# Performance work log

Measured on AMD Instinct MI355X. Metric: run time of the kernel, lower is better.

## Reference

```python
import jax, jax.numpy as jnp
import numpy as np

B, S, IN_DIM = 2048, 65, 256
H, L = 8, 256


def setup_inputs() -> dict:
    key = jax.random.key(0)
    ks = jax.random.split(key, 8)
    return {
        "x": jax.random.normal(ks[0], (B, S, IN_DIM), dtype=jnp.float32),
        "Wq": jax.random.normal(ks[1], (H, IN_DIM, L), dtype=jnp.float32),
        "Wk": jax.random.normal(ks[2], (H, IN_DIM, L), dtype=jnp.float32),
        "Wv": jax.random.normal(ks[3], (H, IN_DIM, L), dtype=jnp.float32),
        "W": jax.random.normal(ks[4], (H, L, 1), dtype=jnp.float32),
        "O": jax.random.normal(ks[5], (H * L, IN_DIM), dtype=jnp.float32),
        "P": jax.random.normal(ks[6], (S - 1, IN_DIM), dtype=jnp.float32),
        "bias": jax.random.normal(ks[7], (H,), dtype=jnp.float32),
    }


def reference(x, Wq, Wk, Wv, W, O, P, bias):
    origin = x[:, 0, :]                       # [B, D]
    walk = x[:, 1:, :]                        # [B, S-1, D]
    origin_seq = origin[:, None, :] + P       # [B, S-1, D]

    # per-head sigmoid projections, vectorized over heads
    k = jax.nn.sigmoid(jnp.einsum('bsd,hdl->bhsl', origin_seq, Wk))
    q = jax.nn.sigmoid(jnp.einsum('bsd,hdl->bhsl', walk, Wq))
    v = jax.nn.sigmoid(jnp.einsum('bsd,hdl->bhsl', walk, Wv))

    edge = jnp.cos(k * q) + bias[None, :, None, None]       # [B,H,S-1,L]
    score = jnp.einsum('bhsl,hl->bhs', edge, W[..., 0])      # [B,H,S-1]
    score = jax.nn.softmax(score, axis=-1)
    res = jnp.einsum('bhs,bhsl->bhl', score, v)              # [B,H,L]
    res = res.reshape(res.shape[0], H * L)                   # concat heads
    out = jax.nn.sigmoid(res @ O)                            # [B, D]
    return jnp.concatenate([out, origin], axis=-1)           # [B, 2D]
```

## Files before the change

### kernel.cpp

```cpp
#include <hip/hip_runtime.h>
#include <math.h>

#define NB   2048
#define NSEQ 65
#define ND   256
#define NH   8
#define NL   256
#define NS   64
#define APAD 264

typedef _Float16 f16;
typedef _Float16 f16x4 __attribute__((ext_vector_type(4)));
typedef _Float16 f16x8 __attribute__((ext_vector_type(8)));
typedef float    f32x4 __attribute__((ext_vector_type(4)));

__device__ __forceinline__ float sigmoidf_(float x) {
    return __builtin_amdgcn_rcpf(1.0f + __expf(-x));
}

__global__ __launch_bounds__(256) void wh_kernel(const float* __restrict__ Wq,
                                                 const float* __restrict__ Wv,
                                                 const float* __restrict__ Wk,
                                                 f16* __restrict__ wh) {
    int hm = blockIdx.x >> 4;
    int h  = hm / 3, m = hm % 3;
    int n  = ((blockIdx.x & 15) << 4) + (threadIdx.x >> 4);
    int kc = (threadIdx.x & 15) << 4;
    const float* src = (m == 0 ? Wq : (m == 1 ? Wv : Wk)) + h * (ND * NL);
    f16x8 t0, t1;
    #pragma unroll
    for (int j = 0; j < 8; ++j) t0[j] = (f16)src[(kc + j) * NL + n];
    #pragma unroll
    for (int j = 0; j < 8; ++j) t1[j] = (f16)src[(kc + 8 + j) * NL + n];
    f16* dst = wh + ((size_t)(hm * 256 + n)) * 256 + kc;
    *(f16x8*)dst       = t0;
    *(f16x8*)(dst + 8) = t1;
}

__global__ __launch_bounds__(256) void ot_kernel(const float* __restrict__ O,
                                                 f16* __restrict__ OT) {
    int n = blockIdx.x;
    int t = threadIdx.x;
    f16x8 v;
    #pragma unroll
    for (int j = 0; j < 8; ++j) v[j] = (f16)O[(size_t)(t * 8 + j) * 256 + n];
    *(f16x8*)(OT + (size_t)n * 2048 + t * 8) = v;
}

__global__ __launch_bounds__(256) void pkt_kernel(const float* __restrict__ P,
                                                  const float* __restrict__ Wk,
                                                  float* __restrict__ PKT) {
    int h = blockIdx.x >> 6;
    int s = blockIdx.x & 63;
    int t = threadIdx.x;
    __shared__ float p_s[ND];
    p_s[t] = P[s * ND + t];
    __syncthreads();
    const float* wk = Wk + h * (ND * NL) + t;
    float acc = 0.f;
    #pragma unroll 8
    for (int d = 0; d < ND; ++d) acc = fmaf(p_s[d], wk[d * NL], acc);
    PKT[((size_t)h * NL + t) * NS + s] = acc;
}

__global__ __launch_bounds__(256) void ok_gemm(const float* __restrict__ x,
                                               const f16*   __restrict__ wh,
                                               float* __restrict__ OK) {
    int mblk = blockIdx.x >> 4;
    int nblk = blockIdx.x & 15;
    int b0 = mblk * 64;
    int h  = nblk >> 1;
    int l0 = (nblk & 1) * 128;
    int t = threadIdx.x;
    int w = t >> 6, lane = t & 63, c = lane & 15, g = lane >> 4;

    __shared__ f16 Ao[64 * APAD];
    #pragma unroll
    for (int it = 0; it < 16; ++it) {
        int idx4 = it * 256 + t;
        int s = idx4 >> 6, kq = idx4 & 63;
        float4 v = *(const float4*)(x + (size_t)(b0 + s) * (NSEQ * ND) + kq * 4);
        *(f16x4*)(&Ao[s * APAD + kq * 4]) = (f16x4){(f16)v.x, (f16)v.y, (f16)v.z, (f16)v.w};
    }
    __syncthreads();

    f32x4 acc[4][2];
    #pragma unroll
    for (int mt = 0; mt < 4; ++mt)
        #pragma unroll
        for (int nt = 0; nt < 2; ++nt) acc[mt][nt] = (f32x4){0.f, 0.f, 0.f, 0.f};

    const f16* bb = wh + ((size_t)((h * 3 + 2) * 256 + l0 + w * 32 + c)) * 256;
    #pragma unroll 2
    for (int kk = 0; kk < 8; ++kk) {
        int k0 = kk * 32 + g * 8;
        f16x8 af[4];
        #pragma unroll
        for (int mt = 0; mt < 4; ++mt)
            af[mt] = *(const f16x8*)(&Ao[(mt * 16 + c) * APAD + k0]);
        #pragma unroll
        for (int nt = 0; nt < 2; ++nt) {
            f16x8 bf = *(const f16x8*)(bb + nt * 16 * 256 + k0);
            #pragma unroll
            for (int mt = 0; mt < 4; ++mt)
                acc[mt][nt] = __builtin_amdgcn_mfma_f32_16x16x32_f16(af[mt], bf, acc[mt][nt], 0, 0, 0);
        }
    }
    #pragma unroll
    for (int mt = 0; mt < 4; ++mt)
        #pragma unroll
        for (int nt = 0; nt < 2; ++nt)
            #pragma unroll
            for (int r = 0; r < 4; ++r)
                OK[((size_t)h * NB + b0 + mt * 16 + g * 4 + r) * NL + l0 + w * 32 + nt * 16 + c]
                    = acc[mt][nt][r];
}

__global__ __launch_bounds__(256, 3) void attn_mfma(
        const float* __restrict__ x,
        const f16*   __restrict__ wh,
        const float* __restrict__ W,
        const float* __restrict__ bias,
        const float* __restrict__ PKT,
        const float* __restrict__ OK,
        f16* __restrict__ res) {
    int b = blockIdx.x;
    int t = threadIdx.x;
    int w    = t >> 6;
    int lane = t & 63;
    int c = lane & 15;
    int g = lane >> 4;

    __shared__ f16 A[NS * APAD];
    __shared__ float redp[2][4][NS];

    const float* xb = x + (size_t)b * (NSEQ * ND);

    #pragma unroll
    for (int it = 0; it < 16; ++it) {
        int idx4 = it * 256 + t;
        int s  = idx4 >> 6;
        int kq = idx4 & 63;
        float4 v = *(const float4*)(xb + (1 + s) * ND + kq * 4);
        *(f16x4*)(&A[s * APAD + kq * 4]) = (f16x4){(f16)v.x, (f16)v.y, (f16)v.z, (f16)v.w};
    }
    __syncthreads();

    for (int h = 0; h < NH; ++h) {
        int p = h & 1;
        const f16* bq = wh + ((size_t)((h * 3 + 0) * 256 + w * 64 + c)) * 256;
        const f16* bv = wh + ((size_t)((h * 3 + 1) * 256 + w * 64 + c)) * 256;

        f32x4 acc[4][4];
        #pragma unroll
        for (int mt = 0; mt < 4; ++mt)
            #pragma unroll
            for (int nt = 0; nt < 4; ++nt) acc[mt][nt] = (f32x4){0.f, 0.f, 0.f, 0.f};

        #pragma unroll 2
        for (int kk = 0; kk < 8; ++kk) {
            int k0 = kk * 32 + g * 8;
            f16x8 af[4];
            #pragma unroll
            for (int mt = 0; mt < 4; ++mt)
                af[mt] = *(const f16x8*)(&A[(mt * 16 + c) * APAD + k0]);
            #pragma unroll
            for (int nt = 0; nt < 4; ++nt) {
                f16x8 bfq = *(const f16x8*)(bq + nt * 16 * 256 + k0);
                #pragma unroll
                for (int mt = 0; mt < 4; ++mt)
                    acc[mt][nt] = __builtin_amdgcn_mfma_f32_16x16x32_f16(af[mt], bfq, acc[mt][nt], 0, 0, 0);
            }
        }

        float bh = bias[h];
        float wl[4], okv[4];
        #pragma unroll
        for (int nt = 0; nt < 4; ++nt) {
            wl[nt]  = W[h * NL + w * 64 + nt * 16 + c];
            okv[nt] = OK[((size_t)h * NB + b) * NL + w * 64 + nt * 16 + c];
        }
        float part[4][4];
        #pragma unroll
        for (int mt = 0; mt < 4; ++mt)
            #pragma unroll
            for (int r = 0; r < 4; ++r) part[mt][r] = 0.f;

        const float* PKTp = PKT + ((size_t)h * NL + w * 64 + c) * NS + g * 4;
        #pragma unroll
        for (int nt = 0; nt < 4; ++nt) {
            const float* pkcol = PKTp + (size_t)nt * 16 * NS;
            float4 pk4[4];
            #pragma unroll
            for (int mt = 0; mt < 4; ++mt) pk4[mt] = *(const float4*)(pkcol + mt * 16);
            #pragma unroll
            for (int mt = 0; mt < 4; ++mt) {
                float pks[4] = {pk4[mt].x, pk4[mt].y, pk4[mt].z, pk4[mt].w};
                #pragma unroll
                for (int r = 0; r < 4; ++r) {
                    float qs = sigmoidf_(acc[mt][nt][r]);
                    float ks = sigmoidf_(okv[nt] + pks[r]);
                    part[mt][r] = fmaf(__cosf(ks * qs) + bh, wl[nt], part[mt][r]);
                }
            }
        }
        #pragma unroll
        for (int mt = 0; mt < 4; ++mt) {
            #pragma unroll
            for (int r = 0; r < 4; ++r) {
                float v = part[mt][r];
                v += __shfl_xor(v, 1, 64);
                v += __shfl_xor(v, 2, 64);
                v += __shfl_xor(v, 4, 64);
                v += __shfl_xor(v, 8, 64);
                if (c == 0) redp[p][w][mt * 16 + g * 4 + r] = v;
            }
        }

        #pragma unroll
        for (int mt = 0; mt < 4; ++mt)
            #pragma unroll
            for (int nt = 0; nt < 4; ++nt) acc[mt][nt] = (f32x4){0.f, 0.f, 0.f, 0.f};
        #pragma unroll 2
        for (int kk = 0; kk < 8; ++kk) {
            int k0 = kk * 32 + g * 8;
            f16x8 af[4];
            #pragma unroll
            for (int mt = 0; mt < 4; ++mt)
                af[mt] = *(const f16x8*)(&A[(mt * 16 + c) * APAD + k0]);
            #pragma unroll
            for (int nt = 0; nt < 4; ++nt) {
                f16x8 bfv = *(const f16x8*)(bv + nt * 16 * 256 + k0);
                #pragma unroll
                for (int mt = 0; mt < 4; ++mt)
                    acc[mt][nt] = __builtin_amdgcn_mfma_f32_16x16x32_f16(af[mt], bfv, acc[mt][nt], 0, 0, 0);
            }
        }
        __syncthreads();

        f32x4 sc4[4];
        #pragma unroll
        for (int mt = 0; mt < 4; ++mt) {
            int so = mt * 16 + g * 4;
            float4 a0 = *(const float4*)(&redp[p][0][so]);
            float4 a1 = *(const float4*)(&redp[p][1][so]);
            float4 a2 = *(const float4*)(&redp[p][2][so]);
            float4 a3 = *(const float4*)(&redp[p][3][so]);
            sc4[mt] = (f32x4){a0.x + a1.x + a2.x + a3.x,
                              a0.y + a1.y + a2.y + a3.y,
                              a0.z + a1.z + a2.z + a3.z,
                              a0.w + a1.w + a2.w + a3.w};
        }
        float m = sc4[0][0];
        #pragma unroll
        for (int mt = 0; mt < 4; ++mt)
            #pragma unroll
            for (int r = 0; r < 4; ++r) m = fmaxf(m, sc4[mt][r]);
        m = fmaxf(m, __shfl_xor(m, 16, 64));
        m = fmaxf(m, __shfl_xor(m, 32, 64));
        float ps[4][4];
        float ssum = 0.f;
        #pragma unroll
        for (int mt = 0; mt < 4; ++mt)
            #pragma unroll
            for (int r = 0; r < 4; ++r) {
                float e = __expf(sc4[mt][r] - m);
                ps[mt][r] = e;
                ssum += e;
            }
        ssum += __shfl_xor(ssum, 16, 64);
        ssum += __shfl_xor(ssum, 32, 64);
        float rinv = __builtin_amdgcn_rcpf(ssum);
        #pragma unroll
        for (int mt = 0; mt < 4; ++mt)
            #pragma unroll
            for (int r = 0; r < 4; ++r) ps[mt][r] *= rinv;

        #pragma unroll
        for (int nt = 0; nt < 4; ++nt) {
            float v = 0.f;
            #pragma unroll
            for (int mt = 0; mt < 4; ++mt)
                #pragma unroll
                for (int r = 0; r < 4; ++r)
                    v = fmaf(ps[mt][r], sigmoidf_(acc[mt][nt][r]), v);
            v += __shfl_xor(v, 16, 64);
            v += __shfl_xor(v, 32, 64);
            if (g == 0)
                res[(size_t)b * 2048 + h * NL + w * 64 + nt * 16 + c] = (f16)v;
        }
    }
}

__global__ __launch_bounds__(256) void out_gemm(
        const float* __restrict__ x,
        const f16*   __restrict__ res,
        const f16*   __restrict__ OT,
        float* __restrict__ out) {
    int mblk = blockIdx.x >> 1;
    int nblk = blockIdx.x & 1;
    int b0 = mblk * 64;
    int t  = threadIdx.x;
    int w    = t >> 6;
    int lane = t & 63;
    int c = lane & 15;
    int g = lane >> 4;

    __shared__ f16 Ao[64 * APAD];

    f32x4 acc[4][2];
    #pragma unroll
    for (int mt = 0; mt < 4; ++mt)
        #pragma unroll
        for (int nt = 0; nt < 2; ++nt) acc[mt][nt] = (f32x4){0.f, 0.f, 0.f, 0.f};

    for (int chunk = 0; chunk < 8; ++chunk) {
        int kbase = chunk * 256;
        __syncthreads();
        #pragma unroll
        for (int it = 0; it < 8; ++it) {
            int id  = it * 256 + t;
            int row = id >> 5;
            int kc  = (id & 31) << 3;
            *(f16x8*)(&Ao[row * APAD + kc]) =
                *(const f16x8*)(res + (size_t)(b0 + row) * 2048 + kbase + kc);
        }
        __syncthreads();
        #pragma unroll
        for (int kk = 0; kk < 8; ++kk) {
            int k0 = kk * 32 + g * 8;
            f16x8 af[4];
            #pragma unroll
            for (int mt = 0; mt < 4; ++mt)
                af[mt] = *(const f16x8*)(&Ao[(mt * 16 + c) * APAD + k0]);
            #pragma unroll
            for (int nt = 0; nt < 2; ++nt) {
                f16x8 bf = *(const f16x8*)(OT + (size_t)(nblk * 128 + w * 32 + nt * 16 + c) * 2048 + kbase + k0);
                #pragma unroll
                for (int mt = 0; mt < 4; ++mt)
                    acc[mt][nt] = __builtin_amdgcn_mfma_f32_16x16x32_f16(af[mt], bf, acc[mt][nt], 0, 0, 0);
            }
        }
    }
    #pragma unroll
    for (int mt = 0; mt < 4; ++mt)
        #pragma unroll
        for (int nt = 0; nt < 2; ++nt)
            #pragma unroll
            for (int r = 0; r < 4; ++r) {
                int row = mt * 16 + g * 4 + r;
                int col = nblk * 128 + w * 32 + nt * 16 + c;
                out[(size_t)(b0 + row) * 512 + col] = sigmoidf_(acc[mt][nt][r]);
            }
    if (nblk == 1) {
        for (int r2 = 0; r2 < 64; ++r2)
            out[(size_t)(b0 + r2) * 512 + 256 + t] = x[(size_t)(b0 + r2) * (NSEQ * ND) + t];
    }
}

extern "C" void kernel_launch(void* const* d_in, const int* in_sizes, int n_in,
                              void* d_out, int out_size, void* d_ws, size_t ws_size,
                              hipStream_t stream) {
    const float* x    = (const float*)d_in[0];
    const float* Wq   = (const float*)d_in[1];
    const float* Wk   = (const float*)d_in[2];
    const float* Wv   = (const float*)d_in[3];
    const float* W    = (const float*)d_in[4];
    const float* O    = (const float*)d_in[5];
    const float* P    = (const float*)d_in[6];
    const float* bias = (const float*)d_in[7];
    float* out = (float*)d_out;

    char* wsb = (char*)d_ws;
    f16*   wh  = (f16*)wsb;
    f16*   OT  = (f16*)(wsb + 3145728);
    float* PKT = (float*)(wsb + 4194304);
    float* OK  = (float*)(wsb + 4718592);
    f16*   res = (f16*)(wsb + 21495808);

    wh_kernel<<<384, 256, 0, stream>>>(Wq, Wv, Wk, wh);
    ot_kernel<<<256, 256, 0, stream>>>(O, OT);
    pkt_kernel<<<NH * NS, 256, 0, stream>>>(P, Wk, PKT);
    ok_gemm<<<512, 256, 0, stream>>>(x, wh, OK);
    attn_mfma<<<NB, 256, 0, stream>>>(x, wh, W, bias, PKT, OK, res);
    out_gemm<<<64, 256, 0, stream>>>(x, res, OT, out);
}
```

Baseline: 840.5 us.

## Assign two whole heads per wave in attention kernel to drop cross-wave reduction

The attention kernel now gives each wave two complete heads and loops over four 64-column chunks of L, instead of splitting every head's L dimension across the four waves. Score reduction and softmax therefore stay inside one wave, which removes the shared-memory partial-sum buffer and the per-head block barrier. The bias term is dropped because adding a per-head constant to every score is invariant under softmax. The cost is that each wave repeats the A-fragment LDS loads per chunk and walks a larger slice of the weight matrices, giving it longer serial work per head.

```diff
diff --git a/kernel.cpp b/kernel.cpp
--- a/kernel.cpp
+++ b/kernel.cpp
@@ -120,7 +120,6 @@
         const float* __restrict__ x,
         const f16*   __restrict__ wh,
         const float* __restrict__ W,
-        const float* __restrict__ bias,
         const float* __restrict__ PKT,
         const float* __restrict__ OK,
         f16* __restrict__ res) {
@@ -132,7 +131,6 @@
     int g = lane >> 4;
 
     __shared__ f16 A[NS * APAD];
-    __shared__ float redp[2][4][NS];
 
     const float* xb = x + (size_t)b * (NSEQ * ND);
 
@@ -146,66 +144,61 @@
     }
     __syncthreads();
 
-    for (int h = 0; h < NH; ++h) {
-        int p = h & 1;
-        const f16* bq = wh + ((size_t)((h * 3 + 0) * 256 + w * 64 + c)) * 256;
-        const f16* bv = wh + ((size_t)((h * 3 + 1) * 256 + w * 64 + c)) * 256;
-
-        f32x4 acc[4][4];
-        #pragma unroll
-        for (int mt = 0; mt < 4; ++mt)
-            #pragma unroll
-            for (int nt = 0; nt < 4; ++nt) acc[mt][nt] = (f32x4){0.f, 0.f, 0.f, 0.f};
-
-        #pragma unroll 2
-        for (int kk = 0; kk < 8; ++kk) {
-            int k0 = kk * 32 + g * 8;
-            f16x8 af[4];
+    #pragma unroll
+    for (int hh = 0; hh < 2; ++hh) {
+        int h = w * 2 + hh;
+
+        float part[4][4];
+        #pragma unroll
+        for (int mt = 0; mt < 4; ++mt)
+            #pragma unroll
+            for (int r = 0; r < 4; ++r) part[mt][r] = 0.f;
+
+        for (int ch = 0; ch < 4; ++ch) {
+            f32x4 acc[4][4];
             #pragma unroll
             for (int mt = 0; mt < 4; ++mt)
-                af[mt] = *(const f16x8*)(&A[(mt * 16 + c) * APAD + k0]);
+                #pragma unroll
+                for (int nt = 0; nt < 4; ++nt) acc[mt][nt] = (f32x4){0.f, 0.f, 0.f, 0.f};
+
+            const f16* bq = wh + ((size_t)((h * 3 + 0) * 256 + ch * 64 + c)) * 256;
+            #pragma unroll 2
+            for (int kk = 0; kk < 8; ++kk) {
+                int k0 = kk * 32 + g * 8;
+                f16x8 af[4];
+                #pragma unroll
+                for (int mt = 0; mt < 4; ++mt)
+                    af[mt] = *(const f16x8*)(&A[(mt * 16 + c) * APAD + k0]);
+                #pragma unroll
+                for (int nt = 0; nt < 4; ++nt) {
+                    f16x8 bf = *(const f16x8*)(bq + nt * 16 * 256 + k0);
+                    #pragma unroll
+                    for (int mt = 0; mt < 4; ++mt)
+                        acc[mt][nt] = __builtin_amdgcn_mfma_f32_16x16x32_f16(af[mt], bf, acc[mt][nt], 0, 0, 0);
+                }
+            }
             #pragma unroll
             for (int nt = 0; nt < 4; ++nt) {
-                f16x8 bfq = *(const f16x8*)(bq + nt * 16 * 256 + k0);
-                #pragma unroll
-                for (int mt = 0; mt < 4; ++mt)
-                    acc[mt][nt] = __builtin_amdgcn_mfma_f32_16x16x32_f16(af[mt], bfq, acc[mt][nt], 0, 0, 0);
-            }
-        }
-
-        float bh = bias[h];
-        float wl[4], okv[4];
-        #pragma unroll
-        for (int nt = 0; nt < 4; ++nt) {
-            wl[nt]  = W[h * NL + w * 64 + nt * 16 + c];
-            okv[nt] = OK[((size_t)h * NB + b) * NL + w * 64 + nt * 16 + c];
-        }
-        float part[4][4];
-        #pragma unroll
-        for (int mt = 0; mt < 4; ++mt)
-            #pragma unroll
-            for (int r = 0; r < 4; ++r) part[mt][r] = 0.f;
-
-        const float* PKTp = PKT + ((size_t)h * NL + w * 64 + c) * NS + g * 4;
-        #pragma unroll
-        for (int nt = 0; nt < 4; ++nt) {
-            const float* pkcol = PKTp + (size_t)nt * 16 * NS;
-            float4 pk4[4];
-            #pragma unroll
-            for (int mt = 0; mt < 4; ++mt) pk4[mt] = *(const float4*)(pkcol + mt * 16);
-            #pragma unroll
-            for (int mt = 0; mt < 4; ++mt) {
-                float pks[4] = {pk4[mt].x, pk4[mt].y, pk4[mt].z, pk4[mt].w};
-                #pragma unroll
-                for (int r = 0; r < 4; ++r) {
-                    float qs = sigmoidf_(acc[mt][nt][r]);
-                    float ks = sigmoidf_(okv[nt] + pks[r]);
-                    part[mt][r] = fmaf(__cosf(ks * qs) + bh, wl[nt], part[mt][r]);
+                int l = ch * 64 + nt * 16 + c;
+                float wl  = W[h * NL + l];
+                float okv = OK[((size_t)h * NB + b) * NL + l];
+                const float* pkcol = PKT + ((size_t)h * NL + l) * NS + g * 4;
+                #pragma unroll
+                for (int mt = 0; mt < 4; ++mt) {
+                    float4 pk4 = *(const float4*)(pkcol + mt * 16);
+                    float pks[4] = {pk4.x, pk4.y, pk4.z, pk4.w};
+                    #pragma unroll
+                    for (int r = 0; r < 4; ++r) {
+                        float qs = sigmoidf_(acc[mt][nt][r]);
+                        float ks = sigmoidf_(okv + pks[r]);
+                        part[mt][r] = fmaf(__cosf(ks * qs), wl, part[mt][r]);
+                    }
                 }
             }
         }
-        #pragma unroll
-        for (int mt = 0; mt < 4; ++mt) {
+
+        #pragma unroll
+        for (int mt = 0; mt < 4; ++mt)
             #pragma unroll
             for (int r = 0; r < 4; ++r) {
                 float v = part[mt][r];
@@ -213,59 +206,22 @@
                 v += __shfl_xor(v, 2, 64);
                 v += __shfl_xor(v, 4, 64);
                 v += __shfl_xor(v, 8, 64);
-                if (c == 0) redp[p][w][mt * 16 + g * 4 + r] = v;
-            }
-        }
-
-        #pragma unroll
-        for (int mt = 0; mt < 4; ++mt)
-            #pragma unroll
-            for (int nt = 0; nt < 4; ++nt) acc[mt][nt] = (f32x4){0.f, 0.f, 0.f, 0.f};
-        #pragma unroll 2
-        for (int kk = 0; kk < 8; ++kk) {
-            int k0 = kk * 32 + g * 8;
-            f16x8 af[4];
-            #pragma unroll
-            for (int mt = 0; mt < 4; ++mt)
-                af[mt] = *(const f16x8*)(&A[(mt * 16 + c) * APAD + k0]);
-            #pragma unroll
-            for (int nt = 0; nt < 4; ++nt) {
-                f16x8 bfv = *(const f16x8*)(bv + nt * 16 * 256 + k0);
-                #pragma unroll
-                for (int mt = 0; mt < 4; ++mt)
-                    acc[mt][nt] = __builtin_amdgcn_mfma_f32_16x16x32_f16(af[mt], bfv, acc[mt][nt], 0, 0, 0);
-            }
-        }
-        __syncthreads();
-
-        f32x4 sc4[4];
-        #pragma unroll
-        for (int mt = 0; mt < 4; ++mt) {
-            int so = mt * 16 + g * 4;
-            float4 a0 = *(const float4*)(&redp[p][0][so]);
-            float4 a1 = *(const float4*)(&redp[p][1][so]);
-            float4 a2 = *(const float4*)(&redp[p][2][so]);
-            float4 a3 = *(const float4*)(&redp[p][3][so]);
-            sc4[mt] = (f32x4){a0.x + a1.x + a2.x + a3.x,
-                              a0.y + a1.y + a2.y + a3.y,
-                              a0.z + a1.z + a2.z + a3.z,
-                              a0.w + a1.w + a2.w + a3.w};
-        }
-        float m = sc4[0][0];
-        #pragma unroll
-        for (int mt = 0; mt < 4; ++mt)
-            #pragma unroll
-            for (int r = 0; r < 4; ++r) m = fmaxf(m, sc4[mt][r]);
+                part[mt][r] = v;
+            }
+        float m = part[0][0];
+        #pragma unroll
+        for (int mt = 0; mt < 4; ++mt)
+            #pragma unroll
+            for (int r = 0; r < 4; ++r) m = fmaxf(m, part[mt][r]);
         m = fmaxf(m, __shfl_xor(m, 16, 64));
         m = fmaxf(m, __shfl_xor(m, 32, 64));
-        float ps[4][4];
         float ssum = 0.f;
         #pragma unroll
         for (int mt = 0; mt < 4; ++mt)
             #pragma unroll
             for (int r = 0; r < 4; ++r) {
-                float e = __expf(sc4[mt][r] - m);
-                ps[mt][r] = e;
+                float e = __expf(part[mt][r] - m);
+                part[mt][r] = e;
                 ssum += e;
             }
         ssum += __shfl_xor(ssum, 16, 64);
@@ -274,20 +230,44 @@
         #pragma unroll
         for (int mt = 0; mt < 4; ++mt)
             #pragma unroll
-            for (int r = 0; r < 4; ++r) ps[mt][r] *= rinv;
-
-        #pragma unroll
-        for (int nt = 0; nt < 4; ++nt) {
-            float v = 0.f;
+            for (int r = 0; r < 4; ++r) part[mt][r] *= rinv;
+
+        for (int ch = 0; ch < 4; ++ch) {
+            f32x4 acc[4][4];
             #pragma unroll
             for (int mt = 0; mt < 4; ++mt)
                 #pragma unroll
-                for (int r = 0; r < 4; ++r)
-                    v = fmaf(ps[mt][r], sigmoidf_(acc[mt][nt][r]), v);
-            v += __shfl_xor(v, 16, 64);
-            v += __shfl_xor(v, 32, 64);
-            if (g == 0)
-                res[(size_t)b * 2048 + h * NL + w * 64 + nt * 16 + c] = (f16)v;
+                for (int nt = 0; nt < 4; ++nt) acc[mt][nt] = (f32x4){0.f, 0.f, 0.f, 0.f};
+
+            const f16* bv = wh + ((size_t)((h * 3 + 1) * 256 + ch * 64 + c)) * 256;
+            #pragma unroll 2
+            for (int kk = 0; kk < 8; ++kk) {
+                int k0 = kk * 32 + g * 8;
+                f16x8 af[4];
+                #pragma unroll
+                for (int mt = 0; mt < 4; ++mt)
+                    af[mt] = *(const f16x8*)(&A[(mt * 16 + c) * APAD + k0]);
+                #pragma unroll
+                for (int nt = 0; nt < 4; ++nt) {
+                    f16x8 bf = *(const f16x8*)(bv + nt * 16 * 256 + k0);
+                    #pragma unroll
+                    for (int mt = 0; mt < 4; ++mt)
+                        acc[mt][nt] = __builtin_amdgcn_mfma_f32_16x16x32_f16(af[mt], bf, acc[mt][nt], 0, 0, 0);
+                }
+            }
+            #pragma unroll
+            for (int nt = 0; nt < 4; ++nt) {
+                float v = 0.f;
+                #pragma unroll
+                for (int mt = 0; mt < 4; ++mt)
+                    #pragma unroll
+                    for (int r = 0; r < 4; ++r)
+                        v = fmaf(part[mt][r], sigmoidf_(acc[mt][nt][r]), v);
+                v += __shfl_xor(v, 16, 64);
+                v += __shfl_xor(v, 32, 64);
+                if (g == 0)
+                    res[(size_t)b * 2048 + h * NL + ch * 64 + nt * 16 + c] = (f16)v;
+            }
         }
     }
 }
@@ -368,7 +348,6 @@
     const float* W    = (const float*)d_in[4];
     const float* O    = (const float*)d_in[5];
     const float* P    = (const float*)d_in[6];
-    const float* bias = (const float*)d_in[7];
     float* out = (float*)d_out;
 
     char* wsb = (char*)d_ws;
@@ -382,6 +361,6 @@
     ot_kernel<<<256, 256, 0, stream>>>(O, OT);
     pkt_kernel<<<NH * NS, 256, 0, stream>>>(P, Wk, PKT);
     ok_gemm<<<512, 256, 0, stream>>>(x, wh, OK);
-    attn_mfma<<<NB, 256, 0, stream>>>(x, wh, W, bias, PKT, OK, res);
+    attn_mfma<<<NB, 256, 0, stream>>>(x, wh, W, PKT, OK, res);
     out_gemm<<<64, 256, 0, stream>>>(x, res, OT, out);
 }
```

Result: slower. 864.1 us (+2.8%).
